# Kernel tuning notes

Measured on AMD Instinct MI355X. Metric: run time of the kernel, lower is better.

## Reference

```python
import jax, jax.numpy as jnp
import numpy as np

D = 1024
N_A = 4096
N_V = 4096


def setup_inputs() -> dict:
    key = jax.random.key(0)
    ks = jax.random.split(key, 6)
    s = 1.0 / np.sqrt(D)  # like torch Linear default init scale
    return {
        "inputs_a": jax.random.normal(ks[0], (N_A, D), dtype=jnp.float32),
        "inputs_v": jax.random.normal(ks[1], (N_V, D), dtype=jnp.float32),
        "W_Ba": jax.random.uniform(ks[2], (D, D), jnp.float32, -s, s),
        "W_Aa": jax.random.uniform(ks[3], (D, D), jnp.float32, -s, s),
        "W_Bv": jax.random.uniform(ks[4], (D, D), jnp.float32, -s, s),
        "W_Av": jax.random.uniform(ks[5], (D, D), jnp.float32, -s, s),
    }


def reference(inputs_a, inputs_v, W_Ba, W_Aa, W_Bv, W_Av):
    # torch Linear: y = x @ W.T ; weights stored [out, in]
    a_a = inputs_a @ W_Aa.T                      # [N_a, D]
    b_a = inputs_a @ W_Ba.T                      # [N_a, D]
    a_v = inputs_v @ W_Av.T                      # [N_v, D]
    b_v = inputs_v @ W_Bv.T                      # [N_v, D]
    scores = b_a @ a_v.T                         # [N_a, N_v]
    alpha_av = jax.nn.softmax(scores, axis=1)    # softmax over N_v
    att_avv = alpha_av @ b_v                     # [N_a, D]
    att_vaa = alpha_av.T @ a_a                   # [N_v, D]
    feature_map_a = att_avv + inputs_a
    feature_map_v = att_vaa + inputs_v
    return feature_map_a, feature_map_v
```

## Files before the change

kernel.cpp:

```cpp
#include <hip/hip_runtime.h>
#include <stdint.h>

#define D_DIM 1024
#define NA_DIM 4096
#define NV_DIM 4096

typedef __bf16 bf16_t;
typedef __bf16 bf16x8 __attribute__((ext_vector_type(8)));
typedef float f32x4 __attribute__((ext_vector_type(4)));

__device__ __forceinline__ void gload_lds16(const void* g, void* lds) {
  __builtin_amdgcn_global_load_lds(
      (const __attribute__((address_space(1))) unsigned int*)g,
      (__attribute__((address_space(3))) unsigned int*)lds, 16, 0, 0);
}

#define VMW(N) asm volatile("s_waitcnt vmcnt(" #N ")" ::: "memory")
#define LKW(N) asm volatile("s_waitcnt lgkmcnt(" #N ")" ::: "memory")
#define BAR() asm volatile("s_barrier" ::: "memory")

__device__ __forceinline__ void gemm256_loose(const bf16_t* __restrict__ A,
                                              const bf16_t* __restrict__ B,
                                              int K, int kb, int klen, int bm, int bn,
                                              bf16_t* lds, f32x4 acc[8][4]) {
  const int tid = threadIdx.x;
  const int lane = tid & 63;
  const int wid = tid >> 6;
  const int wm = wid >> 2;
  const int wn = wid & 3;
  const int frow = lane & 15;
  const int hi = lane >> 4;
  const int k0e = ((hi ^ (frow & 7)) << 3);

  const int sr = (wid << 4) + (lane >> 3);
  const int sc = (((lane & 7) ^ (lane >> 3)) << 3);
  const bf16_t* pAs = A + (size_t)(bm + sr) * K + kb + sc;
  const bf16_t* pBs = B + (size_t)(bn + sr) * K + kb + sc;
  const int dstW = wid << 10;

  const int aBase = (wm << 13) + frow * 64 + k0e;
  const int bBase = 16384 + ((wn >> 1) << 13) + ((wn & 1) << 12) + frow * 64 + k0e;

#define STG_A(kt, h, bufb) do { \
    const bf16_t* s_ = pAs + (size_t)((h) * 128) * K + (size_t)(kt) * 64; \
    bf16_t* d_ = lds + (bufb) * 32768 + (h) * 8192 + dstW; \
    gload_lds16(s_, d_); gload_lds16(s_ + (size_t)8 * K, d_ + 512); } while (0)
#define STG_B(kt, h, bufb) do { \
    const bf16_t* s_ = pBs + (size_t)((h) * 128) * K + (size_t)(kt) * 64; \
    bf16_t* d_ = lds + (bufb) * 32768 + 16384 + (h) * 8192 + dstW; \
    gload_lds16(s_, d_); gload_lds16(s_ + (size_t)8 * K, d_ + 512); } while (0)

#define MFMA(a, b, c) __builtin_amdgcn_mfma_f32_16x16x32_bf16((a), (b), (c), 0, 0, 0)

#define TILE(P, T) do { \
    if ((T) + 1 < NT) { \
      STG_A((T) + 1, 0, (P) ^ 1); STG_A((T) + 1, 1, (P) ^ 1); \
      STG_B((T) + 1, 0, (P) ^ 1); STG_B((T) + 1, 1, (P) ^ 1); \
    } \
    { \
      const bf16_t* Lb_ = lds + (P) * 32768; \
      bf16x8 bf0[4], bf1[4]; \
      _Pragma("unroll") for (int fc = 0; fc < 4; ++fc) { \
        bf0[fc] = *(const bf16x8*)&Lb_[bBase + fc * 1024]; \
        bf1[fc] = *(const bf16x8*)&Lb_[(bBase ^ 32) + fc * 1024]; \
      } \
      _Pragma("unroll") for (int q = 0; q < 4; ++q) { \
        bf16x8 a0 = *(const bf16x8*)&Lb_[aBase + q * 2048]; \
        bf16x8 a1 = *(const bf16x8*)&Lb_[(aBase ^ 32) + q * 2048]; \
        bf16x8 a2 = *(const bf16x8*)&Lb_[aBase + q * 2048 + 1024]; \
        bf16x8 a3 = *(const bf16x8*)&Lb_[(aBase ^ 32) + q * 2048 + 1024]; \
        _Pragma("unroll") for (int fc = 0; fc < 4; ++fc) { \
          acc[q * 2][fc]     = MFMA(a0, bf0[fc], acc[q * 2][fc]); \
          acc[q * 2][fc]     = MFMA(a1, bf1[fc], acc[q * 2][fc]); \
          acc[q * 2 + 1][fc] = MFMA(a2, bf0[fc], acc[q * 2 + 1][fc]); \
          acc[q * 2 + 1][fc] = MFMA(a3, bf1[fc], acc[q * 2 + 1][fc]); \
        } \
      } \
    } \
    LKW(0); VMW(0); BAR(); \
  } while (0)

  const int NT = klen >> 6;

  STG_A(0, 0, 0); STG_A(0, 1, 0); STG_B(0, 0, 0); STG_B(0, 1, 0);
  VMW(0);
  BAR();

  for (int it = 0; it < (NT >> 1); ++it) {
    TILE(0, 2 * it);
    TILE(1, 2 * it + 1);
  }
#undef TILE
#undef MFMA
#undef STG_A
#undef STG_B
}

template <int BF16OUT>
__device__ __forceinline__ void store256(void* Cv, int ldc, int bm, int bn, f32x4 acc[8][4]) {
  const int lane = threadIdx.x & 63;
  const int wid = threadIdx.x >> 6;
  const int wm = wid >> 2, wn = wid & 3;
  const int frow = lane & 15, hi = lane >> 4;
  const int row0 = bm + wm * 128 + hi * 4;
  const int col0 = bn + wn * 64 + frow;
#pragma unroll
  for (int rf = 0; rf < 8; ++rf)
#pragma unroll
    for (int fc = 0; fc < 4; ++fc)
#pragma unroll
      for (int r = 0; r < 4; ++r) {
        size_t idx = (size_t)(row0 + rf * 16 + r) * ldc + (col0 + fc * 16);
        if constexpr (BF16OUT) ((bf16_t*)Cv)[idx] = (bf16_t)acc[rf][fc][r];
        else ((float*)Cv)[idx] = acc[rf][fc][r];
      }
}

__global__ __launch_bounds__(512, 1) void gemm_proj4(
    const bf16_t* __restrict__ Xa, const bf16_t* __restrict__ Xv,
    const bf16_t* __restrict__ W0, const bf16_t* __restrict__ W1,
    const bf16_t* __restrict__ W2, const bf16_t* __restrict__ W3,
    bf16_t* __restrict__ C0, bf16_t* __restrict__ C1,
    bf16_t* __restrict__ C2, bf16_t* __restrict__ C3) {
  __shared__ bf16_t lds[65536];
  const int z = blockIdx.z;
  const bf16_t* A = (z < 2) ? Xa : Xv;
  const bf16_t* B = (z == 0) ? W0 : (z == 1) ? W1 : (z == 2) ? W2 : W3;
  bf16_t* C = (z == 0) ? C0 : (z == 1) ? C1 : (z == 2) ? C2 : C3;
  f32x4 acc[8][4] = {};
  gemm256_loose(A, B, D_DIM, 0, D_DIM, blockIdx.x * 256, blockIdx.y * 256, lds, acc);
  store256<1>(C, D_DIM, blockIdx.x * 256, blockIdx.y * 256, acc);
}

__global__ __launch_bounds__(512, 1) void gemm_scores(const bf16_t* __restrict__ A,
                                                      const bf16_t* __restrict__ B,
                                                      float* __restrict__ C) {
  __shared__ bf16_t lds[65536];
  f32x4 acc[8][4] = {};
  gemm256_loose(A, B, D_DIM, 0, D_DIM, blockIdx.x * 256, blockIdx.y * 256, lds, acc);
  store256<0>(C, NV_DIM, blockIdx.x * 256, blockIdx.y * 256, acc);
}

__global__ __launch_bounds__(512, 1) void gemm_splitk(
    const bf16_t* __restrict__ alpha, const bf16_t* __restrict__ bvT,
    const bf16_t* __restrict__ alphaT, const bf16_t* __restrict__ aaT,
    float* __restrict__ P) {
  __shared__ bf16_t lds[65536];
  const int z = blockIdx.z;
  const bf16_t* A = (z < 2) ? alpha : alphaT;
  const bf16_t* B = (z < 2) ? bvT : aaT;
  const int kb = (z & 1) * 2048;
  f32x4 acc[8][4] = {};
  gemm256_loose(A, B, 4096, kb, 2048, blockIdx.x * 256, blockIdx.y * 256, lds, acc);
  store256<0>(P + (size_t)z * NA_DIM * D_DIM, D_DIM, blockIdx.x * 256, blockIdx.y * 256, acc);
}

__global__ __launch_bounds__(256) void reduce_splitk(const float* __restrict__ P,
                                                     const float* __restrict__ resA,
                                                     const float* __restrict__ resV,
                                                     float* __restrict__ out) {
  const int g = blockIdx.y;
  const size_t n = (size_t)NA_DIM * D_DIM;
  size_t i = ((size_t)blockIdx.x * 256 + threadIdx.x) * 4;
  const float* p0 = P + (size_t)g * 2 * n;
  const float* p1 = p0 + n;
  const float* r = g ? resV : resA;
  float4 a = *(const float4*)(p0 + i);
  float4 b = *(const float4*)(p1 + i);
  float4 c = *(const float4*)(r + i);
  float4 o = {a.x + b.x + c.x, a.y + b.y + c.y, a.z + b.z + c.z, a.w + b.w + c.w};
  *(float4*)(out + g * n + i) = o;
}

__device__ __forceinline__ void cvt8(const float* in, bf16_t* out, int i) {
  float4 v0 = *(const float4*)(in + i);
  float4 v1 = *(const float4*)(in + i + 4);
  bf16x8 o;
  o[0] = (bf16_t)v0.x; o[1] = (bf16_t)v0.y; o[2] = (bf16_t)v0.z; o[3] = (bf16_t)v0.w;
  o[4] = (bf16_t)v1.x; o[5] = (bf16_t)v1.y; o[6] = (bf16_t)v1.z; o[7] = (bf16_t)v1.w;
  *(bf16x8*)(out + i) = o;
}

__global__ __launch_bounds__(256) void cvt2(const float* __restrict__ inA,
                                            const float* __restrict__ inV,
                                            bf16_t* __restrict__ oA,
                                            bf16_t* __restrict__ oV) {
  const float* in = blockIdx.y ? inV : inA;
  bf16_t* out = blockIdx.y ? oV : oA;
  cvt8(in, out, (blockIdx.x * 256 + threadIdx.x) * 8);
}

__global__ __launch_bounds__(256) void cvt4(const float* __restrict__ i0, const float* __restrict__ i1,
                                            const float* __restrict__ i2, const float* __restrict__ i3,
                                            bf16_t* __restrict__ o0, bf16_t* __restrict__ o1,
                                            bf16_t* __restrict__ o2, bf16_t* __restrict__ o3) {
  const int z = blockIdx.y;
  const float* in = (z == 0) ? i0 : (z == 1) ? i1 : (z == 2) ? i2 : i3;
  bf16_t* out = (z == 0) ? o0 : (z == 1) ? o1 : (z == 2) ? o2 : o3;
  cvt8(in, out, (blockIdx.x * 256 + threadIdx.x) * 8);
}

__global__ __launch_bounds__(256) void softmax_rows(const float* __restrict__ S,
                                                    bf16_t* __restrict__ P) {
  const int row = blockIdx.x;
  const int ncol = 4096;
  const float* s = S + (size_t)row * ncol;
  const int base = threadIdx.x * 16;
  float v[16];
  float4* vp = (float4*)v;
#pragma unroll
  for (int q = 0; q < 4; ++q) vp[q] = *(const float4*)(s + base + q * 4);
  float m = v[0];
#pragma unroll
  for (int q = 1; q < 16; ++q) m = fmaxf(m, v[q]);
  for (int off = 32; off; off >>= 1) m = fmaxf(m, __shfl_xor(m, off));
  __shared__ float sm[4], ss[4];
  const int wid = threadIdx.x >> 6, lane = threadIdx.x & 63;
  if (lane == 0) sm[wid] = m;
  __syncthreads();
  m = fmaxf(fmaxf(sm[0], sm[1]), fmaxf(sm[2], sm[3]));
  float sum = 0.f;
#pragma unroll
  for (int q = 0; q < 16; ++q) { v[q] = __expf(v[q] - m); sum += v[q]; }
  for (int off = 32; off; off >>= 1) sum += __shfl_xor(sum, off);
  if (lane == 0) ss[wid] = sum;
  __syncthreads();
  const float inv = 1.0f / (ss[0] + ss[1] + ss[2] + ss[3]);
  bf16x8 o0, o1;
#pragma unroll
  for (int q = 0; q < 8; ++q) { o0[q] = (bf16_t)(v[q] * inv); o1[q] = (bf16_t)(v[q + 8] * inv); }
  bf16_t* p = P + (size_t)row * ncol + base;
  *(bf16x8*)p = o0;
  *(bf16x8*)(p + 8) = o1;
}

__global__ __launch_bounds__(256) void transpose_bf16(const bf16_t* __restrict__ in,
                                                      bf16_t* __restrict__ out, int R, int C) {
  __shared__ bf16_t t[64][72];
  const int bx = blockIdx.x * 64;
  const int by = blockIdx.y * 64;
  const int tid = threadIdx.x;
  const int c8 = (tid & 7) * 8;
  const int r = tid >> 3;
#pragma unroll
  for (int rr = 0; rr < 64; rr += 32) {
    bf16x8 v = *(const bf16x8*)(in + (size_t)(by + r + rr) * C + bx + c8);
    *(bf16x8*)&t[r + rr][c8] = v;
  }
  __syncthreads();
#pragma unroll
  for (int rr = 0; rr < 64; rr += 32) {
    bf16x8 v;
#pragma unroll
    for (int q = 0; q < 8; ++q) v[q] = t[c8 + q][r + rr];
    *(bf16x8*)(out + (size_t)(bx + r + rr) * R + by + c8) = v;
  }
}

extern "C" void kernel_launch(void* const* d_in, const int* in_sizes, int n_in,
                              void* d_out, int out_size, void* d_ws, size_t ws_size,
                              hipStream_t stream) {
  (void)in_sizes; (void)n_in; (void)out_size; (void)ws_size;
  const float* inA = (const float*)d_in[0];
  const float* inV = (const float*)d_in[1];
  const float* wBa = (const float*)d_in[2];
  const float* wAa = (const float*)d_in[3];
  const float* wBv = (const float*)d_in[4];
  const float* wAv = (const float*)d_in[5];
  float* out = (float*)d_out;

  char* w = (char*)d_ws;
  auto take = [&](size_t bytes) { void* p = (void*)w; w += bytes; return p; };
  const size_t XB = (size_t)NA_DIM * D_DIM * 2;
  const size_t WB = (size_t)D_DIM * D_DIM * 2;
  bf16_t* XaB = (bf16_t*)take(XB);
  bf16_t* XvB = (bf16_t*)take(XB);
  bf16_t* WBaB = (bf16_t*)take(WB);
  bf16_t* WAaB = (bf16_t*)take(WB);
  bf16_t* WBvB = (bf16_t*)take(WB);
  bf16_t* WAvB = (bf16_t*)take(WB);
  bf16_t* b_a = (bf16_t*)take(XB);
  bf16_t* a_v = (bf16_t*)take(XB);
  bf16_t* a_a = (bf16_t*)take(XB);
  bf16_t* b_v = (bf16_t*)take(XB);
  bf16_t* a_aT = (bf16_t*)take(XB);
  bf16_t* b_vT = (bf16_t*)take(XB);
  float* scores = (float*)take((size_t)NA_DIM * NV_DIM * 4);
  bf16_t* alpha = (bf16_t*)take((size_t)NA_DIM * NV_DIM * 2);
  bf16_t* alphaT = (bf16_t*)take((size_t)NA_DIM * NV_DIM * 2);
  float* P = scores;

  cvt2<<<dim3(NA_DIM * D_DIM / 2048, 2), 256, 0, stream>>>(inA, inV, XaB, XvB);
  cvt4<<<dim3(D_DIM * D_DIM / 2048, 4), 256, 0, stream>>>(wBa, wAa, wAv, wBv,
                                                          WBaB, WAaB, WAvB, WBvB);

  gemm_proj4<<<dim3(NA_DIM / 256, D_DIM / 256, 4), 512, 0, stream>>>(
      XaB, XvB, WBaB, WAaB, WAvB, WBvB, b_a, a_a, a_v, b_v);

  gemm_scores<<<dim3(NA_DIM / 256, NV_DIM / 256), 512, 0, stream>>>(b_a, a_v, scores);

  softmax_rows<<<NA_DIM, 256, 0, stream>>>(scores, alpha);

  transpose_bf16<<<dim3(NV_DIM / 64, NA_DIM / 64), 256, 0, stream>>>(alpha, alphaT, NA_DIM, NV_DIM);
  transpose_bf16<<<dim3(D_DIM / 64, NA_DIM / 64), 256, 0, stream>>>(a_a, a_aT, NA_DIM, D_DIM);
  transpose_bf16<<<dim3(D_DIM / 64, NV_DIM / 64), 256, 0, stream>>>(b_v, b_vT, NV_DIM, D_DIM);

  gemm_splitk<<<dim3(NA_DIM / 256, D_DIM / 256, 4), 512, 0, stream>>>(
      alpha, b_vT, alphaT, a_aT, P);
  reduce_splitk<<<dim3(NA_DIM * D_DIM / 1024, 2), 256, 0, stream>>>(P, inA, inV, out);
}
```

Before: 209.7 us.

## Write transposed projections directly and fuse split-K reduction via atomic tickets

```diff
diff --git a/kernel.cpp b/kernel.cpp
--- a/kernel.cpp
+++ b/kernel.cpp
@@ -6,6 +6,7 @@
 #define NV_DIM 4096
 
 typedef __bf16 bf16_t;
+typedef __bf16 bf16x4 __attribute__((ext_vector_type(4)));
 typedef __bf16 bf16x8 __attribute__((ext_vector_type(8)));
 typedef float f32x4 __attribute__((ext_vector_type(4)));
 
@@ -116,20 +117,41 @@
       }
 }
 
+__device__ __forceinline__ void store256T(bf16_t* CT, int ldcT, int bm, int bn, f32x4 acc[8][4]) {
+  const int lane = threadIdx.x & 63;
+  const int wid = threadIdx.x >> 6;
+  const int wm = wid >> 2, wn = wid & 3;
+  const int frow = lane & 15, hi = lane >> 4;
+  const int row0 = bm + wm * 128 + hi * 4;
+  const int col0 = bn + wn * 64 + frow;
+#pragma unroll
+  for (int rf = 0; rf < 8; ++rf)
+#pragma unroll
+    for (int fc = 0; fc < 4; ++fc) {
+      bf16x4 v;
+#pragma unroll
+      for (int r = 0; r < 4; ++r) v[r] = (bf16_t)acc[rf][fc][r];
+      *(bf16x4*)(&CT[(size_t)(col0 + fc * 16) * ldcT + row0 + rf * 16]) = v;
+    }
+}
+
 __global__ __launch_bounds__(512, 1) void gemm_proj4(
     const bf16_t* __restrict__ Xa, const bf16_t* __restrict__ Xv,
     const bf16_t* __restrict__ W0, const bf16_t* __restrict__ W1,
     const bf16_t* __restrict__ W2, const bf16_t* __restrict__ W3,
-    bf16_t* __restrict__ C0, bf16_t* __restrict__ C1,
-    bf16_t* __restrict__ C2, bf16_t* __restrict__ C3) {
+    bf16_t* __restrict__ C0, bf16_t* __restrict__ C1T,
+    bf16_t* __restrict__ C2, bf16_t* __restrict__ C3T) {
   __shared__ bf16_t lds[65536];
   const int z = blockIdx.z;
   const bf16_t* A = (z < 2) ? Xa : Xv;
   const bf16_t* B = (z == 0) ? W0 : (z == 1) ? W1 : (z == 2) ? W2 : W3;
-  bf16_t* C = (z == 0) ? C0 : (z == 1) ? C1 : (z == 2) ? C2 : C3;
   f32x4 acc[8][4] = {};
-  gemm256_loose(A, B, D_DIM, 0, D_DIM, blockIdx.x * 256, blockIdx.y * 256, lds, acc);
-  store256<1>(C, D_DIM, blockIdx.x * 256, blockIdx.y * 256, acc);
+  const int bm = blockIdx.x * 256, bn = blockIdx.y * 256;
+  gemm256_loose(A, B, D_DIM, 0, D_DIM, bm, bn, lds, acc);
+  if (z == 0) store256<1>(C0, D_DIM, bm, bn, acc);
+  else if (z == 1) store256T(C1T, NA_DIM, bm, bn, acc);
+  else if (z == 2) store256<1>(C2, D_DIM, bm, bn, acc);
+  else store256T(C3T, NV_DIM, bm, bn, acc);
 }
 
 __global__ __launch_bounds__(512, 1) void gemm_scores(const bf16_t* __restrict__ A,
@@ -144,33 +166,48 @@
 __global__ __launch_bounds__(512, 1) void gemm_splitk(
     const bf16_t* __restrict__ alpha, const bf16_t* __restrict__ bvT,
     const bf16_t* __restrict__ alphaT, const bf16_t* __restrict__ aaT,
-    float* __restrict__ P) {
+    float* __restrict__ P, unsigned* __restrict__ ticket,
+    const float* __restrict__ resA, const float* __restrict__ resV,
+    float* __restrict__ out) {
   __shared__ bf16_t lds[65536];
+  __shared__ unsigned tkOld;
   const int z = blockIdx.z;
   const bf16_t* A = (z < 2) ? alpha : alphaT;
   const bf16_t* B = (z < 2) ? bvT : aaT;
   const int kb = (z & 1) * 2048;
+  const int bm = blockIdx.x * 256, bn = blockIdx.y * 256;
   f32x4 acc[8][4] = {};
-  gemm256_loose(A, B, 4096, kb, 2048, blockIdx.x * 256, blockIdx.y * 256, lds, acc);
-  store256<0>(P + (size_t)z * NA_DIM * D_DIM, D_DIM, blockIdx.x * 256, blockIdx.y * 256, acc);
-}
-
-__global__ __launch_bounds__(256) void reduce_splitk(const float* __restrict__ P,
-                                                     const float* __restrict__ resA,
-                                                     const float* __restrict__ resV,
-                                                     float* __restrict__ out) {
-  const int g = blockIdx.y;
-  const size_t n = (size_t)NA_DIM * D_DIM;
-  size_t i = ((size_t)blockIdx.x * 256 + threadIdx.x) * 4;
-  const float* p0 = P + (size_t)g * 2 * n;
-  const float* p1 = p0 + n;
-  const float* r = g ? resV : resA;
-  float4 a = *(const float4*)(p0 + i);
-  float4 b = *(const float4*)(p1 + i);
-  float4 c = *(const float4*)(r + i);
-  float4 o = {a.x + b.x + c.x, a.y + b.y + c.y, a.z + b.z + c.z, a.w + b.w + c.w};
-  *(float4*)(out + g * n + i) = o;
-}
+  gemm256_loose(A, B, 4096, kb, 2048, bm, bn, lds, acc);
+
+  store256<0>(P + (size_t)z * NA_DIM * D_DIM, D_DIM, bm, bn, acc);
+  __threadfence();
+  if (threadIdx.x == 0)
+    tkOld = atomicAdd(&ticket[(z >> 1) * 64 + blockIdx.x * 4 + blockIdx.y], 1u);
+  __syncthreads();
+  if (tkOld == 1u) {
+    __threadfence();
+    const float* other = P + (size_t)(z ^ 1) * NA_DIM * D_DIM;
+    const float* res = (z >> 1) ? resV : resA;
+    float* o = out + (size_t)(z >> 1) * NA_DIM * D_DIM;
+    const int lane = threadIdx.x & 63;
+    const int wid = threadIdx.x >> 6;
+    const int wm = wid >> 2, wn = wid & 3;
+    const int frow = lane & 15, hi = lane >> 4;
+    const int row0 = bm + wm * 128 + hi * 4;
+    const int col0 = bn + wn * 64 + frow;
+#pragma unroll
+    for (int rf = 0; rf < 8; ++rf)
+#pragma unroll
+      for (int fc = 0; fc < 4; ++fc)
+#pragma unroll
+        for (int r = 0; r < 4; ++r) {
+          size_t idx = (size_t)(row0 + rf * 16 + r) * D_DIM + (col0 + fc * 16);
+          o[idx] = (other[idx] + acc[rf][fc][r]) + res[idx];
+        }
+  }
+}
+
+__global__ void zero_tickets(unsigned* __restrict__ t) { t[threadIdx.x] = 0u; }
 
 __device__ __forceinline__ void cvt8(const float* in, bf16_t* out, int i) {
   float4 v0 = *(const float4*)(in + i);
@@ -281,31 +318,28 @@
   bf16_t* WAvB = (bf16_t*)take(WB);
   bf16_t* b_a = (bf16_t*)take(XB);
   bf16_t* a_v = (bf16_t*)take(XB);
-  bf16_t* a_a = (bf16_t*)take(XB);
-  bf16_t* b_v = (bf16_t*)take(XB);
   bf16_t* a_aT = (bf16_t*)take(XB);
   bf16_t* b_vT = (bf16_t*)take(XB);
   float* scores = (float*)take((size_t)NA_DIM * NV_DIM * 4);
   bf16_t* alpha = (bf16_t*)take((size_t)NA_DIM * NV_DIM * 2);
   bf16_t* alphaT = (bf16_t*)take((size_t)NA_DIM * NV_DIM * 2);
+  unsigned* tickets = (unsigned*)take(1024);
   float* P = scores;
 
+  zero_tickets<<<1, 128, 0, stream>>>(tickets);
   cvt2<<<dim3(NA_DIM * D_DIM / 2048, 2), 256, 0, stream>>>(inA, inV, XaB, XvB);
   cvt4<<<dim3(D_DIM * D_DIM / 2048, 4), 256, 0, stream>>>(wBa, wAa, wAv, wBv,
                                                           WBaB, WAaB, WAvB, WBvB);
 
   gemm_proj4<<<dim3(NA_DIM / 256, D_DIM / 256, 4), 512, 0, stream>>>(
-      XaB, XvB, WBaB, WAaB, WAvB, WBvB, b_a, a_a, a_v, b_v);
+      XaB, XvB, WBaB, WAaB, WAvB, WBvB, b_a, a_aT, a_v, b_vT);
 
   gemm_scores<<<dim3(NA_DIM / 256, NV_DIM / 256), 512, 0, stream>>>(b_a, a_v, scores);
 
   softmax_rows<<<NA_DIM, 256, 0, stream>>>(scores, alpha);
 
   transpose_bf16<<<dim3(NV_DIM / 64, NA_DIM / 64), 256, 0, stream>>>(alpha, alphaT, NA_DIM, NV_DIM);
-  transpose_bf16<<<dim3(D_DIM / 64, NA_DIM / 64), 256, 0, stream>>>(a_a, a_aT, NA_DIM, D_DIM);
-  transpose_bf16<<<dim3(D_DIM / 64, NV_DIM / 64), 256, 0, stream>>>(b_v, b_vT, NV_DIM, D_DIM);
 
   gemm_splitk<<<dim3(NA_DIM / 256, D_DIM / 256, 4), 512, 0, stream>>>(
-      alpha, b_vT, alphaT, a_aT, P);
-  reduce_splitk<<<dim3(NA_DIM * D_DIM / 1024, 2), 256, 0, stream>>>(P, inA, inV, out);
-}
+      alpha, b_vT, alphaT, a_aT, P, tickets, inA, inV, out);
+}
```

Measured after the change: 316.1 us. +50.7%, slower.
